# Performance work log

Measured on AMD Instinct MI355X. Metric: run time of the kernel, lower is better.

The kernel has to match this reference:

```python
import jax, jax.numpy as jnp
import numpy as np

EPS = 1e-12

def setup_inputs() -> dict:
    key = jax.random.key(0)
    k1, k2, k3, k4, k5, k6 = jax.random.split(key, 6)
    B, DIM, T = 16, 256, 2048
    K, D = 1024, 64  # num_embeddings, embedding_dim
    N = B * T
    input_data = jax.random.normal(k1, (B, DIM, T), dtype=jnp.float32)
    codebooks = jax.random.normal(k2, (K, D), dtype=jnp.float32)
    W_in = jax.random.normal(k3, (DIM, D), dtype=jnp.float32) / np.sqrt(DIM)
    b_in = jnp.zeros((D,), dtype=jnp.float32)
    W_out = jax.random.normal(k4, (D, DIM), dtype=jnp.float32) / np.sqrt(D)
    b_out = jnp.zeros((DIM,), dtype=jnp.float32)
    random_vector = jax.random.normal(k5, (N, D), dtype=jnp.float32)
    return {"input_data": input_data, "codebooks": codebooks,
            "W_in": W_in, "b_in": b_in, "W_out": W_out, "b_out": b_out,
            "random_vector": random_vector}

def reference(input_data, codebooks, W_in, b_in, W_out, b_out, random_vector):
    B, DIM, T = input_data.shape
    D = codebooks.shape[1]
    # encode: [B, DIM, T] -> [B, T, DIM] -> project -> [B*T, D]
    x = jnp.einsum('bct,cd->btd', input_data, W_in) + b_in
    x = x.reshape(-1, D)  # [N, D]
    distances = (jnp.sum(x * x, axis=1, keepdims=True)
                 - 2.0 * (x @ codebooks.T)
                 + jnp.sum(codebooks * codebooks, axis=1)[None, :])  # [N, K]
    min_indices = jnp.argmin(distances, axis=1)  # [N]
    hard = codebooks[min_indices]  # [N, D]
    # noise substitution
    norm_resid = jnp.sqrt(jnp.sum((x - hard) ** 2, axis=1, keepdims=True))
    norm_rand = jnp.sqrt(jnp.sum(random_vector ** 2, axis=1, keepdims=True))
    vq_error = (norm_resid / (norm_rand + EPS)) * random_vector
    q = x + vq_error  # [N, D]
    # decode: [N, D] -> [B, T, D] -> project_out -> [B, DIM, T]
    q = q.reshape(B, T, D)
    out = jnp.einsum('btd,dc->bct', q, W_out) + b_out[None, :, None]
    return out
```

## Files before the change

kernel.cpp:

```cpp
#include <hip/hip_runtime.h>
#include <hip/hip_bf16.h>

typedef __bf16 bf16x8 __attribute__((ext_vector_type(8)));
typedef unsigned short u16x8 __attribute__((ext_vector_type(8)));
typedef unsigned int u32x2 __attribute__((ext_vector_type(2)));
typedef unsigned int u32x4 __attribute__((ext_vector_type(4)));
typedef float f32x4 __attribute__((ext_vector_type(4)));
typedef unsigned short u16;

constexpr int DIMc = 256, Tt = 2048, Dd = 64;

__device__ __forceinline__ u16 f2b(float f) {
  unsigned u = __float_as_uint(f);
  return (u16)((u + 0x7FFFu + ((u >> 16) & 1u)) >> 16);
}
__device__ __forceinline__ float b2f(u16 v) {
  return __uint_as_float(((unsigned)v) << 16);
}
__device__ __forceinline__ unsigned f2b2(float a, float b) {
  return (unsigned)f2b(a) | ((unsigned)f2b(b) << 16);
}
__device__ __forceinline__ f32x4 mfma16(u16x8 a, u16x8 b, f32x4 c) {
  return __builtin_amdgcn_mfma_f32_16x16x32_bf16(
      __builtin_bit_cast(bf16x8, a), __builtin_bit_cast(bf16x8, b), c, 0, 0, 0);
}

__global__ __launch_bounds__(512, 2) void nsvq_fused(
    const float* __restrict__ in, const float* __restrict__ rnd,
    const float* __restrict__ cb, const float* __restrict__ Win,
    const float* __restrict__ bin, const float* __restrict__ Wout,
    const float* __restrict__ bout, float* __restrict__ out) {
  __shared__ u16 sm[69632];
  u16* const WinT = sm;
  u16* const InT  = sm + 18432;
  u16* const WoX  = sm + 18432;
  u16* const Xt   = sm + 51200;
  u16* const Xm   = sm + 59392;
  float* const mnp = (float*)(sm + 67584);

  const int tid  = threadIdx.x;
  const int lane = tid & 63;
  const int w    = tid >> 6;
  const int quad = lane >> 4, col = lane & 15;
  const int b    = blockIdx.x >> 4;
  const int t0   = (blockIdx.x & 15) << 7;
  const int myt  = w * 16 + col;

  {
    const int c = tid & 255, db = tid >> 8;
    #pragma unroll
    for (int k = 0; k < 4; ++k) {
      const int d0 = db * 32 + k * 8;
      const float4* wr = (const float4*)(Win + c * 64 + d0);
      float4 v0 = wr[0], v1 = wr[1];
      u16* dst = WinT + c;
      dst[(d0 + 0) * 288] = f2b(v0.x); dst[(d0 + 1) * 288] = f2b(v0.y);
      dst[(d0 + 2) * 288] = f2b(v0.z); dst[(d0 + 3) * 288] = f2b(v0.w);
      dst[(d0 + 4) * 288] = f2b(v1.x); dst[(d0 + 5) * 288] = f2b(v1.y);
      dst[(d0 + 6) * 288] = f2b(v1.z); dst[(d0 + 7) * 288] = f2b(v1.w);
    }
  }
  {
    const int t = tid & 127, cg = tid >> 7;
    const float* ib = in + (size_t)b * DIMc * Tt + t0 + t;
    #pragma unroll
    for (int it = 0; it < 8; ++it) {
      const int c0 = cg * 8 + it * 32;
      u32x4 pk;
      #pragma unroll
      for (int jj = 0; jj < 4; ++jj)
        pk[jj] = f2b2(ib[(size_t)(c0 + 2 * jj) * Tt], ib[(size_t)(c0 + 2 * jj + 1) * Tt]);
      *(u32x4*)(InT + t * 256 + (((c0 >> 3) ^ (t & 7)) << 3)) = pk;
    }
  }
  float rr2v = 0.f;
  const float* rb = rnd + ((size_t)b * Tt + t0) * Dd;
  #pragma unroll
  for (int tt = 0; tt < 16; ++tt) {
    float v = rb[(size_t)(w * 16 + tt) * Dd + lane];
    float s = v * v;
    s += __shfl_xor(s, 1);  s += __shfl_xor(s, 2);  s += __shfl_xor(s, 4);
    s += __shfl_xor(s, 8);  s += __shfl_xor(s, 16); s += __shfl_xor(s, 32);
    if (col == tt) rr2v = s;
  }
  __syncthreads();

  f32x4 acc[4];
  {
    u16x8 Bf[8];
    #pragma unroll
    for (int kt = 0; kt < 8; ++kt)
      Bf[kt] = *(const u16x8*)(InT + myt * 256 + (((kt * 4 + quad) ^ (myt & 7)) << 3));
    #pragma unroll
    for (int mt = 0; mt < 4; ++mt) {
      float4 bi = *(const float4*)(bin + mt * 16 + quad * 4);
      f32x4 a = {bi.x, bi.y, bi.z, bi.w};
      #pragma unroll
      for (int kt = 0; kt < 8; ++kt) {
        u16x8 A = *(const u16x8*)(WinT + (mt * 16 + col) * 288 + kt * 32 + quad * 8);
        a = mfma16(A, Bf[kt], a);
      }
      acc[mt] = a;
    }
  }
  float x2v = 0.f;
  #pragma unroll
  for (int mt = 0; mt < 4; ++mt) {
    #pragma unroll
    for (int r = 0; r < 4; ++r) x2v = fmaf(acc[mt][r], acc[mt][r], x2v);
    u32x2 px = { f2b2(acc[mt][0], acc[mt][1]), f2b2(acc[mt][2], acc[mt][3]) };
    u32x2 pm = { f2b2(-2.f * acc[mt][0], -2.f * acc[mt][1]),
                 f2b2(-2.f * acc[mt][2], -2.f * acc[mt][3]) };
    const int bk  = mt * 2 + (quad >> 1);
    const int off = myt * 64 + ((bk ^ (myt & 7)) << 3) + (quad & 1) * 4;
    *(u32x2*)(Xt + off) = px;
    *(u32x2*)(Xm + off) = pm;
  }
  x2v += __shfl_xor(x2v, 16);
  x2v += __shfl_xor(x2v, 32);
  __syncthreads();

  {
    const int c = tid & 255, db = tid >> 8;
    #pragma unroll
    for (int k = 0; k < 4; ++k) {
      const int d0 = db * 32 + k * 8;
      u32x4 pk;
      #pragma unroll
      for (int jj = 0; jj < 4; ++jj)
        pk[jj] = f2b2(Wout[(size_t)(d0 + 2 * jj) * 256 + c],
                      Wout[(size_t)(d0 + 2 * jj + 1) * 256 + c]);
      *(u32x4*)(WoX + c * 72 + d0) = pk;
    }
  }
  u16x8 Xa[8], Xb[8];
  #pragma unroll
  for (int nt = 0; nt < 8; ++nt) {
    const int tr = nt * 16 + col;
    Xa[nt] = *(const u16x8*)(Xm + tr * 64 + ((quad ^ (tr & 7)) << 3));
    Xb[nt] = *(const u16x8*)(Xm + tr * 64 + (((4 + quad) ^ (tr & 7)) << 3));
  }
  float minv[8];
  #pragma unroll
  for (int i = 0; i < 8; ++i) minv[i] = 3.4e38f;
  const float* cw = cb + (size_t)(w * 128) * Dd;
  for (int mi = 0; mi < 8; ++mi) {
    const float* cr = cw + (size_t)(mi * 16 + col) * Dd + quad * 8;
    float4 c0 = ((const float4*)cr)[0],        c1 = ((const float4*)cr)[1];
    float4 c2 = ((const float4*)(cr + 32))[0], c3 = ((const float4*)(cr + 32))[1];
    float cnA = fmaf(c0.w, c0.w, fmaf(c0.z, c0.z, fmaf(c0.y, c0.y, c0.x * c0.x)));
    float cnB = fmaf(c1.w, c1.w, fmaf(c1.z, c1.z, fmaf(c1.y, c1.y, c1.x * c1.x)));
    float cnC = fmaf(c2.w, c2.w, fmaf(c2.z, c2.z, fmaf(c2.y, c2.y, c2.x * c2.x)));
    float cnD = fmaf(c3.w, c3.w, fmaf(c3.z, c3.z, fmaf(c3.y, c3.y, c3.x * c3.x)));
    float cn = (cnA + cnB) + (cnC + cnD);
    cn += __shfl_xor(cn, 16); cn += __shfl_xor(cn, 32);
    f32x4 cn4;
    #pragma unroll
    for (int r = 0; r < 4; ++r) cn4[r] = __shfl(cn, quad * 4 + r);
    u32x4 a0 = { f2b2(c0.x, c0.y), f2b2(c0.z, c0.w), f2b2(c1.x, c1.y), f2b2(c1.z, c1.w) };
    u32x4 a1 = { f2b2(c2.x, c2.y), f2b2(c2.z, c2.w), f2b2(c3.x, c3.y), f2b2(c3.z, c3.w) };
    u16x8 A0 = __builtin_bit_cast(u16x8, a0);
    u16x8 A1 = __builtin_bit_cast(u16x8, a1);
    #pragma unroll
    for (int nt = 0; nt < 8; ++nt) {
      f32x4 a = mfma16(A0, Xa[nt], cn4);
      a = mfma16(A1, Xb[nt], a);
      #pragma unroll
      for (int r = 0; r < 4; ++r) minv[nt] = fminf(minv[nt], a[r]);
    }
  }
  #pragma unroll
  for (int nt = 0; nt < 8; ++nt) {
    float m = minv[nt];
    m = fminf(m, __shfl_xor(m, 16));
    m = fminf(m, __shfl_xor(m, 32));
    mnp[w * 128 + nt * 16 + col] = m;
  }
  __syncthreads();

  float mv = 3.4e38f;
  #pragma unroll
  for (int j = 0; j < 8; ++j) mv = fminf(mv, mnp[j * 128 + myt]);
  float r2  = fmaxf(x2v + mv, 0.f);
  float scv = sqrtf(r2) / (sqrtf(rr2v) + 1e-12f);
  #pragma unroll
  for (int tt = 0; tt < 16; ++tt) {
    float s  = __shfl(scv, tt);
    float rv = rb[(size_t)(w * 16 + tt) * Dd + lane];
    const int tr  = w * 16 + tt;
    const int idx = tr * 64 + (((lane >> 3) ^ (tr & 7)) << 3) + (lane & 7);
    Xt[idx] = f2b(fmaf(s, rv, b2f(Xt[idx])));
  }

  u16x8 Q0 = *(const u16x8*)(Xt + myt * 64 + ((quad ^ (myt & 7)) << 3));
  u16x8 Q1 = *(const u16x8*)(Xt + myt * 64 + (((4 + quad) ^ (myt & 7)) << 3));
  float* ob0 = out + (size_t)b * DIMc * Tt + t0 + myt;
  #pragma unroll
  for (int mt = 0; mt < 16; ++mt) {
    const u16* ar = WoX + (mt * 16 + col) * 72;
    u16x8 A0 = *(const u16x8*)(ar + quad * 8);
    u16x8 A1 = *(const u16x8*)(ar + 32 + quad * 8);
    float4 bo = *(const float4*)(bout + mt * 16 + quad * 4);
    f32x4 a = {bo.x, bo.y, bo.z, bo.w};
    a = mfma16(A0, Q0, a);
    a = mfma16(A1, Q1, a);
    float* ob = ob0 + (size_t)(mt * 16 + quad * 4) * Tt;
    #pragma unroll
    for (int r = 0; r < 4; ++r) ob[(size_t)r * Tt] = a[r];
  }
}

extern "C" void kernel_launch(void* const* d_in, const int* in_sizes, int n_in,
                              void* d_out, int out_size, void* d_ws, size_t ws_size,
                              hipStream_t stream) {
  const float *in = nullptr, *cbp = nullptr, *rnd = nullptr, *bin = nullptr, *bout = nullptr;
  const float* w16[2] = {nullptr, nullptr}; int nw = 0;
  for (int i = 0; i < n_in; ++i) {
    switch (in_sizes[i]) {
      case 8388608: in  = (const float*)d_in[i]; break;
      case 65536:   cbp = (const float*)d_in[i]; break;
      case 2097152: rnd = (const float*)d_in[i]; break;
      case 64:      bin = (const float*)d_in[i]; break;
      case 256:     bout= (const float*)d_in[i]; break;
      case 16384:   if (nw < 2) w16[nw++] = (const float*)d_in[i]; break;
      default: break;
    }
  }
  if (!in)   in  = (const float*)d_in[0];
  if (!cbp)  cbp = (const float*)d_in[1];
  if (nw < 2) { w16[0] = (const float*)d_in[2]; w16[1] = (const float*)d_in[4]; }
  if (!bin)  bin = (const float*)d_in[3];
  if (!bout) bout = (const float*)d_in[5];
  if (!rnd)  rnd = (const float*)d_in[6];

  nsvq_fused<<<256, 512, 0, stream>>>(in, rnd, cbp, w16[0], bin, w16[1], bout, (float*)d_out);
}
```

Baseline: 112.4 us.

## Halve tile to 64 timesteps per block, fold -2 into codebook, cache random rows

Each block now handles 64 timesteps with 256 threads across 512 blocks, and each wave scans 256 codebook entries instead of 128. Shared memory drops by reusing the Win region for Wout and dropping the separate -2x buffer; the -2 factor is now applied to the codebook operand during bf16 conversion. Random-vector rows are kept in registers so they are not reloaded from global memory in the noise step. This raises block count and occupancy, but every block now reconverts the full codebook and weights for half as many tokens, doubling that redundant work overall.

```diff
diff --git a/kernel.cpp b/kernel.cpp
--- a/kernel.cpp
+++ b/kernel.cpp
@@ -25,32 +25,31 @@
       __builtin_bit_cast(bf16x8, a), __builtin_bit_cast(bf16x8, b), c, 0, 0, 0);
 }
 
-__global__ __launch_bounds__(512, 2) void nsvq_fused(
+__global__ __launch_bounds__(256, 2) void nsvq_fused(
     const float* __restrict__ in, const float* __restrict__ rnd,
     const float* __restrict__ cb, const float* __restrict__ Win,
     const float* __restrict__ bin, const float* __restrict__ Wout,
     const float* __restrict__ bout, float* __restrict__ out) {
-  __shared__ u16 sm[69632];
+  __shared__ u16 sm[39424];
   u16* const WinT = sm;
+  u16* const WoX  = sm;
   u16* const InT  = sm + 18432;
-  u16* const WoX  = sm + 18432;
-  u16* const Xt   = sm + 51200;
-  u16* const Xm   = sm + 59392;
-  float* const mnp = (float*)(sm + 67584);
+  u16* const Xt   = sm + 34816;
+  float* const mnp = (float*)(sm + 38912);
 
   const int tid  = threadIdx.x;
   const int lane = tid & 63;
   const int w    = tid >> 6;
   const int quad = lane >> 4, col = lane & 15;
-  const int b    = blockIdx.x >> 4;
-  const int t0   = (blockIdx.x & 15) << 7;
+  const int b    = blockIdx.x >> 5;
+  const int t0   = (blockIdx.x & 31) << 6;
   const int myt  = w * 16 + col;
 
   {
-    const int c = tid & 255, db = tid >> 8;
-    #pragma unroll
-    for (int k = 0; k < 4; ++k) {
-      const int d0 = db * 32 + k * 8;
+    const int c = tid;
+    #pragma unroll
+    for (int k = 0; k < 8; ++k) {
+      const int d0 = k * 8;
       const float4* wr = (const float4*)(Win + c * 64 + d0);
       float4 v0 = wr[0], v1 = wr[1];
       u16* dst = WinT + c;
@@ -61,7 +60,7 @@
     }
   }
   {
-    const int t = tid & 127, cg = tid >> 7;
+    const int t = tid & 63, cg = tid >> 6;
     const float* ib = in + (size_t)b * DIMc * Tt + t0 + t;
     #pragma unroll
     for (int it = 0; it < 8; ++it) {
@@ -73,12 +72,12 @@
       *(u32x4*)(InT + t * 256 + (((c0 >> 3) ^ (t & 7)) << 3)) = pk;
     }
   }
-  float rr2v = 0.f;
+  float rr2v = 0.f, rv[16];
   const float* rb = rnd + ((size_t)b * Tt + t0) * Dd;
   #pragma unroll
   for (int tt = 0; tt < 16; ++tt) {
-    float v = rb[(size_t)(w * 16 + tt) * Dd + lane];
-    float s = v * v;
+    rv[tt] = rb[(size_t)(w * 16 + tt) * Dd + lane];
+    float s = rv[tt] * rv[tt];
     s += __shfl_xor(s, 1);  s += __shfl_xor(s, 2);  s += __shfl_xor(s, 4);
     s += __shfl_xor(s, 8);  s += __shfl_xor(s, 16); s += __shfl_xor(s, 32);
     if (col == tt) rr2v = s;
@@ -109,22 +108,19 @@
     #pragma unroll
     for (int r = 0; r < 4; ++r) x2v = fmaf(acc[mt][r], acc[mt][r], x2v);
     u32x2 px = { f2b2(acc[mt][0], acc[mt][1]), f2b2(acc[mt][2], acc[mt][3]) };
-    u32x2 pm = { f2b2(-2.f * acc[mt][0], -2.f * acc[mt][1]),
-                 f2b2(-2.f * acc[mt][2], -2.f * acc[mt][3]) };
     const int bk  = mt * 2 + (quad >> 1);
     const int off = myt * 64 + ((bk ^ (myt & 7)) << 3) + (quad & 1) * 4;
     *(u32x2*)(Xt + off) = px;
-    *(u32x2*)(Xm + off) = pm;
   }
   x2v += __shfl_xor(x2v, 16);
   x2v += __shfl_xor(x2v, 32);
   __syncthreads();
 
   {
-    const int c = tid & 255, db = tid >> 8;
-    #pragma unroll
-    for (int k = 0; k < 4; ++k) {
-      const int d0 = db * 32 + k * 8;
+    const int c = tid;
+    #pragma unroll
+    for (int k = 0; k < 8; ++k) {
+      const int d0 = k * 8;
       u32x4 pk;
       #pragma unroll
       for (int jj = 0; jj < 4; ++jj)
@@ -133,18 +129,18 @@
       *(u32x4*)(WoX + c * 72 + d0) = pk;
     }
   }
-  u16x8 Xa[8], Xb[8];
-  #pragma unroll
-  for (int nt = 0; nt < 8; ++nt) {
+  u16x8 Xa[4], Xb[4];
+  #pragma unroll
+  for (int nt = 0; nt < 4; ++nt) {
     const int tr = nt * 16 + col;
-    Xa[nt] = *(const u16x8*)(Xm + tr * 64 + ((quad ^ (tr & 7)) << 3));
-    Xb[nt] = *(const u16x8*)(Xm + tr * 64 + (((4 + quad) ^ (tr & 7)) << 3));
-  }
-  float minv[8];
-  #pragma unroll
-  for (int i = 0; i < 8; ++i) minv[i] = 3.4e38f;
-  const float* cw = cb + (size_t)(w * 128) * Dd;
-  for (int mi = 0; mi < 8; ++mi) {
+    Xa[nt] = *(const u16x8*)(Xt + tr * 64 + ((quad ^ (tr & 7)) << 3));
+    Xb[nt] = *(const u16x8*)(Xt + tr * 64 + (((4 + quad) ^ (tr & 7)) << 3));
+  }
+  float minv[4];
+  #pragma unroll
+  for (int i = 0; i < 4; ++i) minv[i] = 3.4e38f;
+  const float* cw = cb + (size_t)(w * 256) * Dd;
+  for (int mi = 0; mi < 16; ++mi) {
     const float* cr = cw + (size_t)(mi * 16 + col) * Dd + quad * 8;
     float4 c0 = ((const float4*)cr)[0],        c1 = ((const float4*)cr)[1];
     float4 c2 = ((const float4*)(cr + 32))[0], c3 = ((const float4*)(cr + 32))[1];
@@ -157,12 +153,14 @@
     f32x4 cn4;
     #pragma unroll
     for (int r = 0; r < 4; ++r) cn4[r] = __shfl(cn, quad * 4 + r);
-    u32x4 a0 = { f2b2(c0.x, c0.y), f2b2(c0.z, c0.w), f2b2(c1.x, c1.y), f2b2(c1.z, c1.w) };
-    u32x4 a1 = { f2b2(c2.x, c2.y), f2b2(c2.z, c2.w), f2b2(c3.x, c3.y), f2b2(c3.z, c3.w) };
+    u32x4 a0 = { f2b2(-2.f * c0.x, -2.f * c0.y), f2b2(-2.f * c0.z, -2.f * c0.w),
+                 f2b2(-2.f * c1.x, -2.f * c1.y), f2b2(-2.f * c1.z, -2.f * c1.w) };
+    u32x4 a1 = { f2b2(-2.f * c2.x, -2.f * c2.y), f2b2(-2.f * c2.z, -2.f * c2.w),
+                 f2b2(-2.f * c3.x, -2.f * c3.y), f2b2(-2.f * c3.z, -2.f * c3.w) };
     u16x8 A0 = __builtin_bit_cast(u16x8, a0);
     u16x8 A1 = __builtin_bit_cast(u16x8, a1);
     #pragma unroll
-    for (int nt = 0; nt < 8; ++nt) {
+    for (int nt = 0; nt < 4; ++nt) {
       f32x4 a = mfma16(A0, Xa[nt], cn4);
       a = mfma16(A1, Xb[nt], a);
       #pragma unroll
@@ -170,26 +168,25 @@
     }
   }
   #pragma unroll
-  for (int nt = 0; nt < 8; ++nt) {
+  for (int nt = 0; nt < 4; ++nt) {
     float m = minv[nt];
     m = fminf(m, __shfl_xor(m, 16));
     m = fminf(m, __shfl_xor(m, 32));
-    mnp[w * 128 + nt * 16 + col] = m;
+    mnp[w * 64 + nt * 16 + col] = m;
   }
   __syncthreads();
 
   float mv = 3.4e38f;
   #pragma unroll
-  for (int j = 0; j < 8; ++j) mv = fminf(mv, mnp[j * 128 + myt]);
+  for (int j = 0; j < 4; ++j) mv = fminf(mv, mnp[j * 64 + myt]);
   float r2  = fmaxf(x2v + mv, 0.f);
   float scv = sqrtf(r2) / (sqrtf(rr2v) + 1e-12f);
   #pragma unroll
   for (int tt = 0; tt < 16; ++tt) {
     float s  = __shfl(scv, tt);
-    float rv = rb[(size_t)(w * 16 + tt) * Dd + lane];
     const int tr  = w * 16 + tt;
     const int idx = tr * 64 + (((lane >> 3) ^ (tr & 7)) << 3) + (lane & 7);
-    Xt[idx] = f2b(fmaf(s, rv, b2f(Xt[idx])));
+    Xt[idx] = f2b(fmaf(s, rv[tt], b2f(Xt[idx])));
   }
 
   u16x8 Q0 = *(const u16x8*)(Xt + myt * 64 + ((quad ^ (myt & 7)) << 3));
@@ -233,5 +230,5 @@
   if (!bout) bout = (const float*)d_in[5];
   if (!rnd)  rnd = (const float*)d_in[6];
 
-  nsvq_fused<<<256, 512, 0, stream>>>(in, rnd, cbp, w16[0], bin, w16[1], bout, (float*)d_out);
-}
+  nsvq_fused<<<512, 256, 0, stream>>>(in, rnd, cbp, w16[0], bin, w16[1], bout, (float*)d_out);
+}
```

Measured after the change: 121.6 us. 8.2% more time.
